# Performance work log

Measured on AMD Instinct MI355X. Metric: run time of the kernel, lower is better.

## Reference

```python
import jax, jax.numpy as jnp
import numpy as np

B, H, S, D = 2, 16, 2048, 64
SCALE = 1.0 / (D ** 0.5)
MASK_FILL = -1e9


def setup_inputs() -> dict:
    key = jax.random.key(0)
    kq, kk, kv = jax.random.split(key, 3)
    q = jax.random.normal(kq, (B, H, S, D), dtype=jnp.float32)
    k = jax.random.normal(kk, (B, H, S, D), dtype=jnp.float32)
    v = jax.random.normal(kv, (B, H, S, D), dtype=jnp.float32)
    # causal mask: True where attention is disallowed (j > i)
    attn_mask = jnp.triu(jnp.ones((S, S), dtype=jnp.bool_), k=1)[None, None]
    return {"q": q, "k": k, "v": v, "attn_mask": attn_mask}


def reference(q, k, v, attn_mask):
    # scores: [B,H,S,S] = (q @ k^T) * scale, then masked_fill(mask, -1e9)
    scores = jnp.einsum("bhqd,bhkd->bhqk", q, k) * SCALE
    scores = jnp.where(attn_mask, MASK_FILL, scores)
    attn_prob = jax.nn.softmax(scores, axis=-1)  # dropout p=0.0 (eval)
    context = jnp.einsum("bhqk,bhkd->bhqd", attn_prob, v)
    return (context, attn_prob)
```

## Files before the change

### kernel.cpp

```cpp
#include <hip/hip_runtime.h>

#define NB 2
#define NH 16
#define SS 2048
#define DD 64
constexpr float kScale = 0.125f;

typedef __attribute__((ext_vector_type(8))) short bf16x8;
typedef __attribute__((ext_vector_type(4))) float f32x4;

union FragAB { bf16x8 v; unsigned u[4]; };

__device__ __forceinline__ unsigned pack2bf(float lo, float hi) {
  unsigned ul = __float_as_uint(lo) + 0x8000u;
  unsigned uh = __float_as_uint(hi) + 0x8000u;
  return __builtin_amdgcn_perm(uh, ul, 0x07060302u);
}
__device__ __forceinline__ short f2bf(float f) {
  return (short)((__float_as_uint(f) + 0x8000u) >> 16);
}

struct KC { float4 x[8]; };

__global__ __launch_bounds__(256, 4) void attn_mfma(
    const float* __restrict__ Q, const float* __restrict__ K,
    const float* __restrict__ V, float* __restrict__ ctx,
    float* __restrict__ prob) {
  const int b    = blockIdx.x;
  const int xcd  = b & 7;
  const int slot = b >> 3;
  const int oct  = slot >> 5;
  const int cu5  = slot & 31;
  const int ww   = cu5 & 7;
  const int hl   = cu5 >> 3;
  const int qt   = (3 - oct) * 8 + ((oct & 1) ? (7 - ww) : ww);
  const int bh   = xcd * 4 + hl;

  const int t    = threadIdx.x;
  const int lane = t & 63;
  const int wave = t >> 6;
  const int quad = lane >> 4;
  const int l16  = lane & 15;

  const int q_base = qt * 64;
  const int i_max  = q_base + 63;
  const int qw     = q_base + wave * 16;
  const size_t hoff = (size_t)bh * SS * DD;
  const float* Kh = K + hoff;
  const float* Vh = V + hoff;

  __shared__ __align__(16) short Vt[2][DD][40];
  __shared__ __align__(16) short Pld[4][16][40];
  __shared__ float linv_s[4][20];

  FragAB aq[2];
  {
    const float* qp = Q + hoff + (size_t)(qw + l16) * DD + quad * 8;
#pragma unroll
    for (int c = 0; c < 2; ++c) {
      float4 x = *(const float4*)(qp + c * 32);
      float4 y = *(const float4*)(qp + c * 32 + 4);
      aq[c].u[0] = pack2bf(x.x * kScale, x.y * kScale);
      aq[c].u[1] = pack2bf(x.z * kScale, x.w * kScale);
      aq[c].u[2] = pack2bf(y.x * kScale, y.y * kScale);
      aq[c].u[3] = pack2bf(y.z * kScale, y.w * kScale);
    }
  }

  const int irow0 = qw + quad * 4;
  const int nc = (i_max + 32) >> 5;

  auto kload = [&](KC& kk, int j0) {
    const float* kp = Kh + (size_t)(j0 + l16) * DD + quad * 8;
    kk.x[0] = *(const float4*)(kp);
    kk.x[1] = *(const float4*)(kp + 4);
    kk.x[2] = *(const float4*)(kp + 32);
    kk.x[3] = *(const float4*)(kp + 36);
    kk.x[4] = *(const float4*)(kp + 16 * DD);
    kk.x[5] = *(const float4*)(kp + 16 * DD + 4);
    kk.x[6] = *(const float4*)(kp + 16 * DD + 32);
    kk.x[7] = *(const float4*)(kp + 16 * DD + 36);
  };

  auto qke = [&](const KC& kk, int j0, f32x4 et[2]) {
#pragma unroll
    for (int tl = 0; tl < 2; ++tl) {
      const float4 a  = kk.x[tl * 4 + 0];
      const float4 b2 = kk.x[tl * 4 + 1];
      const float4 cc = kk.x[tl * 4 + 2];
      const float4 d2 = kk.x[tl * 4 + 3];
      FragAB b0, b1;
      b0.u[0] = pack2bf(a.x, a.y);   b0.u[1] = pack2bf(a.z, a.w);
      b0.u[2] = pack2bf(b2.x, b2.y); b0.u[3] = pack2bf(b2.z, b2.w);
      b1.u[0] = pack2bf(cc.x, cc.y); b1.u[1] = pack2bf(cc.z, cc.w);
      b1.u[2] = pack2bf(d2.x, d2.y); b1.u[3] = pack2bf(d2.z, d2.w);
      f32x4 acc = {0.f, 0.f, 0.f, 0.f};
      acc = __builtin_amdgcn_mfma_f32_16x16x32_bf16(aq[0].v, b0.v, acc, 0, 0, 0);
      acc = __builtin_amdgcn_mfma_f32_16x16x32_bf16(aq[1].v, b1.v, acc, 0, 0, 0);
      const int jc = j0 + tl * 16 + l16;
#pragma unroll
      for (int r = 0; r < 4; ++r)
        et[tl][r] = (jc <= irow0 + r) ? __expf(acc[r]) : 0.f;
    }
  };

  const int jj = t >> 3;
  const int d0 = (t & 7) * 8;
  const int cw = jj ^ ((t & 3) << 3);

  f32x4 O[4] = {{0,0,0,0},{0,0,0,0},{0,0,0,0},{0,0,0,0}};
  float l_acc[4] = {0.f, 0.f, 0.f, 0.f};
  float* ppk = prob + (size_t)(bh * SS + qw + l16) * SS;

  {
    const float* vp = Vh + (size_t)jj * DD + d0;
    float4 pv0 = *(const float4*)vp, pv1 = *(const float4*)(vp + 4);
    float tmp[8] = {pv0.x,pv0.y,pv0.z,pv0.w,pv1.x,pv1.y,pv1.z,pv1.w};
#pragma unroll
    for (int i2 = 0; i2 < 8; ++i2) Vt[0][d0 + i2][cw] = f2bf(tmp[i2]);
  }

  KC ka, kb;
  kload(ka, 0);

  auto body = [&](int c, const KC& kc, KC& kn, bool pf) {
    __syncthreads();
    const int cn = c + 1;
    float4 pv0, pv1;
    if (cn < nc) {
      const float* vp = Vh + (size_t)(cn * 32 + jj) * DD + d0;
      pv0 = *(const float4*)vp; pv1 = *(const float4*)(vp + 4);
    }
    if (pf) kload(kn, cn * 32);
    f32x4 et[2];
    qke(kc, c * 32, et);
#pragma unroll
    for (int r = 0; r < 4; ++r) l_acc[r] += et[0][r] + et[1][r];
#pragma unroll
    for (int tl = 0; tl < 2; ++tl)
#pragma unroll
      for (int r = 0; r < 4; ++r)
        Pld[wave][quad * 4 + r][tl * 16 + l16] = f2bf(et[tl][r]);
    FragAB ap;
    ap.v = *(const bf16x8*)&Pld[wave][l16][quad * 8];
    uint4 pk; pk.x = ap.u[0]; pk.y = ap.u[1]; pk.z = ap.u[2]; pk.w = ap.u[3];
    *reinterpret_cast<uint4*>(ppk + c * 16 + quad * 4) = pk;
    const int vb = c & 1;
#pragma unroll
    for (int n = 0; n < 4; ++n) {
      const int dim = n * 16 + l16;
      const int cb = (quad << 3) ^ ((((dim >> 3) & 3)) << 3);
      FragAB bv;
      bv.v = *(const bf16x8*)&Vt[vb][dim][cb];
      O[n] = __builtin_amdgcn_mfma_f32_16x16x32_bf16(ap.v, bv.v, O[n], 0, 0, 0);
    }
    if (cn < nc) {
      float tmp[8] = {pv0.x,pv0.y,pv0.z,pv0.w,pv1.x,pv1.y,pv1.z,pv1.w};
#pragma unroll
      for (int i2 = 0; i2 < 8; ++i2) Vt[cn & 1][d0 + i2][cw] = f2bf(tmp[i2]);
    }
  };

  {
    int c = 0;
    for (; c + 2 <= nc; c += 2) {
      body(c, ka, kb, true);
      body(c + 1, kb, ka, c + 2 < nc);
    }
    if (c < nc) body(c, ka, kb, false);
  }

  float inv_l[4];
#pragma unroll
  for (int r = 0; r < 4; ++r) {
    float s2 = l_acc[r];
    s2 += __shfl_xor(s2, 1, 64);
    s2 += __shfl_xor(s2, 2, 64);
    s2 += __shfl_xor(s2, 4, 64);
    s2 += __shfl_xor(s2, 8, 64);
    inv_l[r] = 1.f / s2;
  }
  if (l16 < 4) linv_s[wave][quad * 4 + l16] = inv_l[l16];

#pragma unroll
  for (int n = 0; n < 4; ++n)
#pragma unroll
    for (int r = 0; r < 4; ++r)
      ctx[(size_t)(bh * SS + irow0 + r) * DD + n * 16 + l16] = O[n][r] * inv_l[r];

  asm volatile("" ::: "memory");
  __builtin_amdgcn_s_waitcnt(0);
  asm volatile("" ::: "memory");

  const int prow = lane & 15;
  const int cg   = lane >> 4;
  const float lv = linv_s[wave][prow];
  float* pr = prob + (size_t)(bh * SS + qw + prow) * SS;
  for (int c = nc - 1; c >= 0; --c) {
    const uint4 pk = *reinterpret_cast<const uint4*>(pr + c * 16 + cg * 4);
    float4 o0, o1;
    o0.x = __uint_as_float(pk.x << 16) * lv;
    o0.y = __uint_as_float(pk.x & 0xffff0000u) * lv;
    o0.z = __uint_as_float(pk.y << 16) * lv;
    o0.w = __uint_as_float(pk.y & 0xffff0000u) * lv;
    o1.x = __uint_as_float(pk.z << 16) * lv;
    o1.y = __uint_as_float(pk.z & 0xffff0000u) * lv;
    o1.z = __uint_as_float(pk.w << 16) * lv;
    o1.w = __uint_as_float(pk.w & 0xffff0000u) * lv;
    *reinterpret_cast<float4*>(pr + c * 32 + cg * 8) = o0;
    *reinterpret_cast<float4*>(pr + c * 32 + cg * 8 + 4) = o1;
  }
  const float4 z4 = {0.f, 0.f, 0.f, 0.f};
  for (int c = nc; c < SS / 32; ++c) {
    *reinterpret_cast<float4*>(pr + c * 32 + cg * 8) = z4;
    *reinterpret_cast<float4*>(pr + c * 32 + cg * 8 + 4) = z4;
  }
}

extern "C" void kernel_launch(void* const* d_in, const int* in_sizes, int n_in,
                              void* d_out, int out_size, void* d_ws, size_t ws_size,
                              hipStream_t stream) {
  const float* q = (const float*)d_in[0];
  const float* k = (const float*)d_in[1];
  const float* v = (const float*)d_in[2];
  float* ctx  = (float*)d_out;
  float* prob = (float*)d_out + (size_t)NB * NH * SS * DD;
  attn_mfma<<<dim3(NB * NH * 32), dim3(256), 0, stream>>>(q, k, v, ctx, prob);
}
```

Before: 878.9 us.

## Recompute QK^T exp in second pass instead of staging bf16 probs in output

Instead of writing unnormalized bf16 probabilities into the prob buffer during the main loop and re-reading them afterwards to normalize, the kernel now reruns the QK^T MFMA and exp in a second pass once the row sums are known, then writes normalized fp32 probabilities directly. This removes the staging writes and read-back of global memory in exchange for reloading K and repeating the QK^T work. Stores of context, probabilities and zero fill now use nontemporal hints. The odd-chunk tail call in the first loop is removed, which relies on nc always being even.

```diff
diff --git a/kernel.cpp b/kernel.cpp
--- a/kernel.cpp
+++ b/kernel.cpp
@@ -110,7 +110,6 @@
 
   f32x4 O[4] = {{0,0,0,0},{0,0,0,0},{0,0,0,0},{0,0,0,0}};
   float l_acc[4] = {0.f, 0.f, 0.f, 0.f};
-  float* ppk = prob + (size_t)(bh * SS + qw + l16) * SS;
 
   {
     const float* vp = Vh + (size_t)jj * DD + d0;
@@ -143,8 +142,6 @@
         Pld[wave][quad * 4 + r][tl * 16 + l16] = f2bf(et[tl][r]);
     FragAB ap;
     ap.v = *(const bf16x8*)&Pld[wave][l16][quad * 8];
-    uint4 pk; pk.x = ap.u[0]; pk.y = ap.u[1]; pk.z = ap.u[2]; pk.w = ap.u[3];
-    *reinterpret_cast<uint4*>(ppk + c * 16 + quad * 4) = pk;
     const int vb = c & 1;
 #pragma unroll
     for (int n = 0; n < 4; ++n) {
@@ -167,7 +164,6 @@
       body(c, ka, kb, true);
       body(c + 1, kb, ka, c + 2 < nc);
     }
-    if (c < nc) body(c, ka, kb, false);
   }
 
   float inv_l[4];
@@ -186,34 +182,48 @@
   for (int n = 0; n < 4; ++n)
 #pragma unroll
     for (int r = 0; r < 4; ++r)
-      ctx[(size_t)(bh * SS + irow0 + r) * DD + n * 16 + l16] = O[n][r] * inv_l[r];
-
-  asm volatile("" ::: "memory");
-  __builtin_amdgcn_s_waitcnt(0);
-  asm volatile("" ::: "memory");
-
-  const int prow = lane & 15;
-  const int cg   = lane >> 4;
-  const float lv = linv_s[wave][prow];
-  float* pr = prob + (size_t)(bh * SS + qw + prow) * SS;
-  for (int c = nc - 1; c >= 0; --c) {
-    const uint4 pk = *reinterpret_cast<const uint4*>(pr + c * 16 + cg * 4);
-    float4 o0, o1;
-    o0.x = __uint_as_float(pk.x << 16) * lv;
-    o0.y = __uint_as_float(pk.x & 0xffff0000u) * lv;
-    o0.z = __uint_as_float(pk.y << 16) * lv;
-    o0.w = __uint_as_float(pk.y & 0xffff0000u) * lv;
-    o1.x = __uint_as_float(pk.z << 16) * lv;
-    o1.y = __uint_as_float(pk.z & 0xffff0000u) * lv;
-    o1.z = __uint_as_float(pk.w << 16) * lv;
-    o1.w = __uint_as_float(pk.w & 0xffff0000u) * lv;
-    *reinterpret_cast<float4*>(pr + c * 32 + cg * 8) = o0;
-    *reinterpret_cast<float4*>(pr + c * 32 + cg * 8 + 4) = o1;
-  }
-  const float4 z4 = {0.f, 0.f, 0.f, 0.f};
+      __builtin_nontemporal_store(
+          O[n][r] * inv_l[r],
+          ctx + (size_t)(bh * SS + irow0 + r) * DD + n * 16 + l16);
+
+  const float lv = linv_s[wave][l16];
+  float* pr2 = prob + (size_t)(bh * SS + qw + l16) * SS;
+
+  kload(ka, 0);
+  for (int c = 0; c < nc; c += 2) {
+    kload(kb, (c + 1) * 32);
+#pragma unroll
+    for (int h = 0; h < 2; ++h) {
+      const KC& kc = h ? kb : ka;
+      const int cc2 = c + h;
+      if (h == 1 && cc2 + 1 < nc) kload(ka, (cc2 + 1) * 32);
+      f32x4 et[2];
+      qke(kc, cc2 * 32, et);
+#pragma unroll
+      for (int tl = 0; tl < 2; ++tl)
+#pragma unroll
+        for (int r = 0; r < 4; ++r)
+          Pld[wave][quad * 4 + r][tl * 16 + l16] = f2bf(et[tl][r]);
+      FragAB ap;
+      ap.v = *(const bf16x8*)&Pld[wave][l16][quad * 8];
+      f32x4 o0, o1;
+      o0[0] = __uint_as_float(ap.u[0] << 16) * lv;
+      o0[1] = __uint_as_float(ap.u[0] & 0xffff0000u) * lv;
+      o0[2] = __uint_as_float(ap.u[1] << 16) * lv;
+      o0[3] = __uint_as_float(ap.u[1] & 0xffff0000u) * lv;
+      o1[0] = __uint_as_float(ap.u[2] << 16) * lv;
+      o1[1] = __uint_as_float(ap.u[2] & 0xffff0000u) * lv;
+      o1[2] = __uint_as_float(ap.u[3] << 16) * lv;
+      o1[3] = __uint_as_float(ap.u[3] & 0xffff0000u) * lv;
+      __builtin_nontemporal_store(o0, (f32x4*)(pr2 + cc2 * 32 + quad * 8));
+      __builtin_nontemporal_store(o1, (f32x4*)(pr2 + cc2 * 32 + quad * 8 + 4));
+    }
+  }
+
+  const f32x4 z4 = {0.f, 0.f, 0.f, 0.f};
   for (int c = nc; c < SS / 32; ++c) {
-    *reinterpret_cast<float4*>(pr + c * 32 + cg * 8) = z4;
-    *reinterpret_cast<float4*>(pr + c * 32 + cg * 8 + 4) = z4;
+    __builtin_nontemporal_store(z4, (f32x4*)(pr2 + c * 32 + quad * 8));
+    __builtin_nontemporal_store(z4, (f32x4*)(pr2 + c * 32 + quad * 8 + 4));
   }
 }
 
```

Result: faster. 819.7 us (-6.7%).
